# Kernel optimization log

Measured on AMD Instinct MI355X. Metric: run time of the kernel, lower is better.

## Reference

```python
import jax, jax.numpy as jnp
import numpy as np

HEAD_DIM = 64
N_HEADS = 64
N_KV = 8
Q_MULT = N_HEADS // N_KV  # 8
HIDDEN = 2880
SEQ = 1024
BATCH = 2
SLIDING_WINDOW = 128  # layer_idx=0 -> window active
ROPE_THETA = 150000.0
SCALING = 32.0
NTK_ALPHA = 1.0
NTK_BETA = 32.0
INIT_CTX = 4096
EPS = 1e-5


def _rope_caches(seq_len):
    # YaRN rotary caches (static numpy precompute, as in the source module)
    steps = np.arange(0, HEAD_DIM, 2, dtype=np.float32)
    freq = np.power(np.float32(ROPE_THETA), steps / np.float32(HEAD_DIM))
    concentration = np.float32(0.1) * np.log(np.float32(SCALING)) + 1.0
    d_half = np.float32(HEAD_DIM / 2.0)
    log_base = np.log(np.float32(ROPE_THETA))
    low = d_half * np.log(np.float32(INIT_CTX) / (np.float32(NTK_BETA) * np.float32(2.0 * np.pi))) / log_base
    high = d_half * np.log(np.float32(INIT_CTX) / (np.float32(NTK_ALPHA) * np.float32(2.0 * np.pi))) / log_base
    ramp = (np.arange(HEAD_DIM // 2, dtype=np.float32) - low) / (high - low)
    mask = 1.0 - np.clip(ramp, 0.0, 1.0)
    inv_freq = (1.0 / (np.float32(SCALING) * freq)) * (1.0 - mask) + (1.0 / freq) * mask
    pos = np.arange(seq_len, dtype=np.float32)
    freqs = np.einsum('i,j->ij', pos, inv_freq.astype(np.float32))
    cos = (np.cos(freqs) * concentration).astype(np.float32)
    sin = (np.sin(freqs) * concentration).astype(np.float32)
    return jnp.asarray(cos), jnp.asarray(sin)


def _apply_rotary(t, cos, sin):
    # t: (B, S, ..., head_dim); cos/sin: (S, head_dim//2). Rotate-half style.
    shape = (1, t.shape[1]) + (1,) * (t.ndim - 3) + (cos.shape[-1],)
    c = cos.reshape(shape)
    s = sin.reshape(shape)
    first, second = jnp.split(t, 2, axis=-1)
    return jnp.concatenate([first * c - second * s, second * c + first * s], axis=-1)


def setup_inputs() -> dict:
    key = jax.random.key(0)
    ks = jax.random.split(key, 6)
    qkv_dim = (N_HEADS + 2 * N_KV) * HEAD_DIM  # 5120
    return {
        'x': jax.random.normal(ks[0], (BATCH, SEQ, HIDDEN), dtype=jnp.float32),
        'norm_w': jnp.ones((HIDDEN,), dtype=jnp.float32),
        'qkv_w': jax.random.normal(ks[1], (qkv_dim, HIDDEN), dtype=jnp.float32) * 0.02,
        'qkv_b': jax.random.normal(ks[2], (qkv_dim,), dtype=jnp.float32) * 0.02,
        'out_w': jax.random.normal(ks[3], (HIDDEN, N_HEADS * HEAD_DIM), dtype=jnp.float32) * 0.02,
        'out_b': jax.random.normal(ks[4], (HIDDEN,), dtype=jnp.float32) * 0.02,
        'sinks': jax.random.normal(ks[5], (N_HEADS,), dtype=jnp.float32),
    }


def reference(x, norm_w, qkv_w, qkv_b, out_w, out_b, sinks):
    B, S, _ = x.shape
    # RMSNorm (fp32 accumulation)
    xf = x.astype(jnp.float32)
    rms = jnp.mean(xf * xf, axis=-1, keepdims=True)
    t = (xf * jax.lax.rsqrt(rms + EPS) * norm_w).astype(x.dtype)
    # QKV projection (fp32 accumulation)
    qkv = jnp.matmul(t.astype(jnp.float32), qkv_w.T) + qkv_b
    q_dim = N_HEADS * HEAD_DIM
    kv_dim = N_KV * HEAD_DIM
    q = qkv[..., :q_dim].reshape(B, S, N_KV, Q_MULT, HEAD_DIM)
    k = qkv[..., q_dim:q_dim + kv_dim].reshape(B, S, N_KV, HEAD_DIM)
    v = qkv[..., q_dim + kv_dim:].reshape(B, S, N_KV, HEAD_DIM)
    # YaRN rotary embedding
    cos, sin = _rope_caches(S)
    q = _apply_rotary(q, cos, sin)
    k = _apply_rotary(k, cos, sin)
    # causal + sliding-window mask
    neg_inf = jnp.float32(-jnp.inf)
    mask = jnp.triu(jnp.full((S, S), neg_inf, dtype=jnp.float32), k=1)
    mask = mask + jnp.tril(jnp.full((S, S), neg_inf, dtype=jnp.float32), k=-SLIDING_WINDOW)
    sm_scale = jnp.float32(1.0 / np.sqrt(HEAD_DIM))
    # GQA attention with sink logits
    logits = jnp.einsum('bqhmd,bkhd->bhmqk', q, k) * sm_scale + mask[None, None, None]
    sink = jnp.broadcast_to(sinks.reshape(1, N_KV, Q_MULT, 1, 1), (B, N_KV, Q_MULT, S, 1))
    logits = jnp.concatenate([logits, sink], axis=-1)
    w = jax.nn.softmax(logits, axis=-1)[..., :-1]  # drop sink column
    attn = jnp.einsum('bhmqk,bkhd->bqhmd', w, v).reshape(B, S, N_HEADS * HEAD_DIM)
    # output projection (fp32 accumulation) + residual
    out = jnp.matmul(attn, out_w.T) + out_b
    return x + out
```

## Files before the change

### kernel.cpp

```cpp
#include <hip/hip_runtime.h>

typedef unsigned short ushort_t;
typedef __attribute__((ext_vector_type(8))) short short8;
typedef __attribute__((ext_vector_type(8))) __bf16 bf16x8;
typedef __attribute__((ext_vector_type(4))) float float4v;
typedef __attribute__((ext_vector_type(4))) unsigned int uint4v;

__device__ __forceinline__ float bf2f(ushort_t u) {
    unsigned int v = ((unsigned int)u) << 16;
    return __builtin_bit_cast(float, v);
}
__device__ __forceinline__ ushort_t f2bf(float f) {
    unsigned int u = __builtin_bit_cast(unsigned int, f);
    unsigned int lsb = (u >> 16) & 1u;
    u += 0x7fffu + lsb;
    return (ushort_t)(u >> 16);
}
__device__ __forceinline__ uint4v pack8(const ushort_t* r) {
    uint4v u;
#pragma unroll
    for (int i = 0; i < 4; ++i)
        u[i] = (unsigned int)r[2 * i] | ((unsigned int)r[2 * i + 1] << 16);
    return u;
}
__device__ __forceinline__ void unpack8(uint4v u, float* f) {
#pragma unroll
    for (int i = 0; i < 4; ++i) {
        unsigned int x = u[i];
        f[2 * i] = __builtin_bit_cast(float, x << 16);
        f[2 * i + 1] = __builtin_bit_cast(float, x & 0xffff0000u);
    }
}
__device__ __forceinline__ uint4v ld8f32_bf(const float* p) {
    float4v a = *(const float4v*)p;
    float4v b = *(const float4v*)(p + 4);
    ushort_t r[8];
#pragma unroll
    for (int j = 0; j < 4; ++j) { r[j] = f2bf(a[j]); r[4 + j] = f2bf(b[j]); }
    return pack8(r);
}

#if __has_builtin(__builtin_amdgcn_global_load_lds)
#define HAVE_GLDS 1
__device__ __forceinline__ void glds16(const ushort_t* gp, ushort_t* lp) {
    __builtin_amdgcn_global_load_lds((const __attribute__((address_space(1))) void*)gp,
                                     (__attribute__((address_space(3))) void*)lp, 16, 0, 0);
}
#else
#define HAVE_GLDS 0
#endif

template <typename V>
__device__ __forceinline__ auto mfma_sel(V a, V b, float4v c, int)
    -> decltype(__builtin_amdgcn_mfma_f32_16x16x32_bf16(a, b, c, 0, 0, 0)) {
    return __builtin_amdgcn_mfma_f32_16x16x32_bf16(a, b, c, 0, 0, 0);
}
template <typename V>
__device__ __forceinline__ float4v mfma_sel(V a, V b, float4v c, long) {
    return __builtin_amdgcn_mfma_f32_16x16x32_bf16(__builtin_bit_cast(bf16x8, a),
                                                   __builtin_bit_cast(bf16x8, b), c, 0, 0, 0);
}
__device__ __forceinline__ float4v mfma_bf16(short8 a, short8 b, float4v c) {
    return mfma_sel(a, b, c, 0);
}

__device__ __forceinline__ float wave_sum(float v) {
#pragma unroll
    for (int o = 32; o; o >>= 1) v += __shfl_xor(v, o);
    return v;
}

#define HIDDEN 2880
#define NTOK 2048
#define QKV_DIM 5120
#define ATTN_DIM 4096
#define SM_SCALE 0.125f

#define ROPE_STEP 0.37244970540869975f
#define ROPE_CONC 1.3465735902799727f
#define ROPE_LOW 8.092890725542669f
#define ROPE_INVDEN 0.10745959154836568f

__device__ __forceinline__ float rope_invfreq(int j) {
    float invf = __expf(-(float)j * ROPE_STEP);
    float ramp = ((float)j - ROPE_LOW) * ROPE_INVDEN;
    float mask = 1.f - fminf(fmaxf(ramp, 0.f), 1.f);
    return invf * ((1.f - mask) * 0.03125f + mask);
}

__global__ __launch_bounds__(256) void prep_kernel(const float* __restrict__ x,
                                                   const float* __restrict__ wgt,
                                                   ushort_t* __restrict__ tout,
                                                   const float* __restrict__ a,
                                                   ushort_t* __restrict__ ao, int na8,
                                                   const float* __restrict__ b,
                                                   ushort_t* __restrict__ bo, int nb8) {
    const int tid = threadIdx.x;
    __shared__ float red[4];
    if (blockIdx.x < NTOK) {
        const int tok = blockIdx.x;
        const float* xr = x + (size_t)tok * HIDDEN;
        float v[16];
        float ss = 0.f;
#pragma unroll
        for (int i = 0; i < 2; ++i) {
            int c = tid + i * 256;
            if (c < 360) {
                float4v va = *(const float4v*)(xr + c * 8);
                float4v vb = *(const float4v*)(xr + c * 8 + 4);
#pragma unroll
                for (int j = 0; j < 4; ++j) { v[i * 8 + j] = va[j]; v[i * 8 + 4 + j] = vb[j]; }
#pragma unroll
                for (int j = 0; j < 8; ++j) ss += v[i * 8 + j] * v[i * 8 + j];
            }
        }
        ss = wave_sum(ss);
        if ((tid & 63) == 0) red[tid >> 6] = ss;
        __syncthreads();
        float scale = rsqrtf((red[0] + red[1] + red[2] + red[3]) * (1.f / 2880.f) + 1e-5f);
#pragma unroll
        for (int i = 0; i < 2; ++i) {
            int c = tid + i * 256;
            if (c < 360) {
                float4v wa = *(const float4v*)(wgt + c * 8);
                float4v wb = *(const float4v*)(wgt + c * 8 + 4);
                ushort_t r[8];
#pragma unroll
                for (int j = 0; j < 4; ++j) {
                    r[j] = f2bf(v[i * 8 + j] * scale * wa[j]);
                    r[4 + j] = f2bf(v[i * 8 + 4 + j] * scale * wb[j]);
                }
                *(uint4v*)(tout + (size_t)tok * HIDDEN + c * 8) = pack8(r);
            }
        }
    } else {
        int idx = (blockIdx.x - NTOK) * 256 + tid;
        if (idx < na8) {
            *(uint4v*)(ao + (size_t)idx * 8) = ld8f32_bf(a + (size_t)idx * 8);
        } else {
            int j = idx - na8;
            if (j < nb8) *(uint4v*)(bo + (size_t)j * 8) = ld8f32_bf(b + (size_t)j * 8);
        }
    }
}

__global__ __launch_bounds__(256) void rmsnorm_kernel(const float* __restrict__ x,
                                                      const float* __restrict__ wgt,
                                                      ushort_t* __restrict__ out) {
    const int tok = blockIdx.x, tid = threadIdx.x;
    const float* xr = x + (size_t)tok * HIDDEN;
    float v[16];
    float ss = 0.f;
#pragma unroll
    for (int i = 0; i < 2; ++i) {
        int c = tid + i * 256;
        if (c < 360) {
            float4v a = *(const float4v*)(xr + c * 8);
            float4v b = *(const float4v*)(xr + c * 8 + 4);
#pragma unroll
            for (int j = 0; j < 4; ++j) { v[i * 8 + j] = a[j]; v[i * 8 + 4 + j] = b[j]; }
#pragma unroll
            for (int j = 0; j < 8; ++j) ss += v[i * 8 + j] * v[i * 8 + j];
        }
    }
    ss = wave_sum(ss);
    __shared__ float red[4];
    if ((tid & 63) == 0) red[tid >> 6] = ss;
    __syncthreads();
    float scale = rsqrtf((red[0] + red[1] + red[2] + red[3]) * (1.f / 2880.f) + 1e-5f);
#pragma unroll
    for (int i = 0; i < 2; ++i) {
        int c = tid + i * 256;
        if (c < 360) {
            float4v wa = *(const float4v*)(wgt + c * 8);
            float4v wb = *(const float4v*)(wgt + c * 8 + 4);
            ushort_t r[8];
#pragma unroll
            for (int j = 0; j < 4; ++j) {
                r[j] = f2bf(v[i * 8 + j] * scale * wa[j]);
                r[4 + j] = f2bf(v[i * 8 + 4 + j] * scale * wb[j]);
            }
            *(uint4v*)(out + (size_t)tok * HIDDEN + c * 8) = pack8(r);
        }
    }
}

template <int BN, bool RESID, bool OUTF32, bool BF16B>
__global__ __launch_bounds__(256) void gemm_kernel(const ushort_t* __restrict__ A,
                                                   const void* __restrict__ B,
                                                   const float* __restrict__ bias,
                                                   const float* __restrict__ resid,
                                                   void* __restrict__ Cout, int M, int N, int K) {
    constexpr int BM = 128, BK = 64;
    constexpr bool GL = BF16B && (HAVE_GLDS != 0);
    constexpr int LDT = GL ? 64 : 72;
    constexpr int NBUF = GL ? 2 : 1;
    static_assert(BN == 160 || BN == 128 || BN == 96 || BN == 64, "");
    __shared__ __align__(16) ushort_t As[NBUF][BM * LDT];
    __shared__ __align__(16) ushort_t Bs[NBUF][BN * LDT];

    const int nbx = gridDim.x;
    int wg = blockIdx.y * nbx + blockIdx.x;
    {
        const int nwg = nbx * gridDim.y;
        const int cpx = nwg >> 3;
        wg = (wg & 7) * cpx + (wg >> 3);
    }
    const int m0 = (wg / nbx) * BM;
    const int n0 = (wg % nbx) * BN;
    const int tid = threadIdx.x;
    const int w = tid >> 6, lane = tid & 63;
    const int quad = lane >> 4, l16 = lane & 15;

    constexpr int WN = BN / 2;
    constexpr int NI = WN / 16;
    const int wm = (w >> 1) * 64;
    const int wn = (w & 1) * WN;

    float4v acc[4][NI];
#pragma unroll
    for (int i = 0; i < 4; ++i)
#pragma unroll
        for (int j = 0; j < NI; ++j) acc[i][j] = (float4v){0.f, 0.f, 0.f, 0.f};

    const int nk = K / BK;

#if HAVE_GLDS
    if constexpr (GL) {
        constexpr int NAI = BM / 32;
        constexpr int NBI = BN / 32;
        const ushort_t* Bp = (const ushort_t*)B;
        const ushort_t* agp[NAI];
        const ushort_t* bgp[NBI];
        ushort_t* alp[2][NAI];
        ushort_t* blp[2][NBI];
#pragma unroll
        for (int i = 0; i < NAI; ++i) {
            int sb = (w * NAI + i) * 64;
            int s = sb + lane, r = s >> 3, p = s & 7, c = p ^ (r & 7);
            agp[i] = A + (size_t)(m0 + r) * K + c * 8;
            alp[0][i] = &As[0][sb * 8];
            alp[1][i] = &As[1][sb * 8];
        }
#pragma unroll
        for (int i = 0; i < NBI; ++i) {
            int sb = (w * NBI + i) * 64;
            int s = sb + lane, r = s >> 3, p = s & 7, c = p ^ (r & 7);
            bgp[i] = Bp + (size_t)(n0 + r) * K + c * 8;
            blp[0][i] = &Bs[0][sb * 8];
            blp[1][i] = &Bs[1][sb * 8];
        }
#pragma unroll
        for (int i = 0; i < NAI; ++i) glds16(agp[i], alp[0][i]);
#pragma unroll
        for (int i = 0; i < NBI; ++i) glds16(bgp[i], blp[0][i]);
        __syncthreads();

        for (int kt = 0; kt < nk; ++kt) {
            const int cur = kt & 1;
            if (kt + 1 < nk) {
                const int k0 = (kt + 1) * BK;
#pragma unroll
                for (int i = 0; i < NAI; ++i) glds16(agp[i] + k0, alp[cur ^ 1][i]);
#pragma unroll
                for (int i = 0; i < NBI; ++i) glds16(bgp[i] + k0, blp[cur ^ 1][i]);
            }
            const ushort_t* Asb = As[cur];
            const ushort_t* Bsb = Bs[cur];
#pragma unroll
            for (int ks = 0; ks < 2; ++ks) {
                short8 af[4], bfr[NI];
#pragma unroll
                for (int mi = 0; mi < 4; ++mi) {
                    int row = wm + mi * 16 + l16;
                    af[mi] = *(const short8*)(Asb + row * LDT + ((ks * 4 + quad) ^ (row & 7)) * 8);
                }
#pragma unroll
                for (int ni = 0; ni < NI; ++ni) {
                    int row = wn + ni * 16 + l16;
                    bfr[ni] = *(const short8*)(Bsb + row * LDT + ((ks * 4 + quad) ^ (row & 7)) * 8);
                }
#pragma unroll
                for (int mi = 0; mi < 4; ++mi)
#pragma unroll
                    for (int ni = 0; ni < NI; ++ni)
                        acc[mi][ni] = mfma_bf16(af[mi], bfr[ni], acc[mi][ni]);
            }
            __syncthreads();
        }
    } else
#endif
    {
        constexpr int ACH = BM * BK / 8 / 256;
        constexpr int BCH = BN * BK / 8 / 256;
        uint4v areg[ACH], breg[BCH];
#pragma unroll
        for (int i = 0; i < ACH; ++i) {
            int c = tid + i * 256, r = c >> 3, col = c & 7;
            areg[i] = *(const uint4v*)(A + (size_t)(m0 + r) * K + col * 8);
        }
#pragma unroll
        for (int i = 0; i < BCH; ++i) {
            int c = tid + i * 256, r = c >> 3, col = c & 7;
            if constexpr (BF16B)
                breg[i] = *(const uint4v*)((const ushort_t*)B + (size_t)(n0 + r) * K + col * 8);
            else
                breg[i] = ld8f32_bf((const float*)B + (size_t)(n0 + r) * K + col * 8);
        }
        for (int kt = 0; kt < nk; ++kt) {
            __syncthreads();
#pragma unroll
            for (int i = 0; i < ACH; ++i) {
                int c = tid + i * 256, r = c >> 3, col = c & 7;
                *(uint4v*)(&As[0][r * LDT + col * 8]) = areg[i];
            }
#pragma unroll
            for (int i = 0; i < BCH; ++i) {
                int c = tid + i * 256, r = c >> 3, col = c & 7;
                *(uint4v*)(&Bs[0][r * LDT + col * 8]) = breg[i];
            }
            __syncthreads();
            if (kt + 1 < nk) {
                const int k0 = (kt + 1) * BK;
#pragma unroll
                for (int i = 0; i < ACH; ++i) {
                    int c = tid + i * 256, r = c >> 3, col = c & 7;
                    areg[i] = *(const uint4v*)(A + (size_t)(m0 + r) * K + k0 + col * 8);
                }
#pragma unroll
                for (int i = 0; i < BCH; ++i) {
                    int c = tid + i * 256, r = c >> 3, col = c & 7;
                    if constexpr (BF16B)
                        breg[i] = *(const uint4v*)((const ushort_t*)B + (size_t)(n0 + r) * K + k0 + col * 8);
                    else
                        breg[i] = ld8f32_bf((const float*)B + (size_t)(n0 + r) * K + k0 + col * 8);
                }
            }
#pragma unroll
            for (int ks = 0; ks < 2; ++ks) {
                short8 af[4], bfr[NI];
#pragma unroll
                for (int mi = 0; mi < 4; ++mi)
                    af[mi] = *(const short8*)(&As[0][(wm + mi * 16 + l16) * LDT + ks * 32 + quad * 8]);
#pragma unroll
                for (int ni = 0; ni < NI; ++ni)
                    bfr[ni] = *(const short8*)(&Bs[0][(wn + ni * 16 + l16) * LDT + ks * 32 + quad * 8]);
#pragma unroll
                for (int mi = 0; mi < 4; ++mi)
#pragma unroll
                    for (int ni = 0; ni < NI; ++ni)
                        acc[mi][ni] = mfma_bf16(af[mi], bfr[ni], acc[mi][ni]);
            }
        }
    }

#pragma unroll
    for (int ni = 0; ni < NI; ++ni) {
        int gc = n0 + wn + ni * 16 + l16;
        float bv = bias[gc];
#pragma unroll
        for (int mi = 0; mi < 4; ++mi) {
#pragma unroll
            for (int r = 0; r < 4; ++r) {
                int gr = m0 + wm + mi * 16 + quad * 4 + r;
                float vv = acc[mi][ni][r] + bv;
                if constexpr (RESID) vv += resid[(size_t)gr * N + gc];
                if constexpr (OUTF32) ((float*)Cout)[(size_t)gr * N + gc] = vv;
                else ((ushort_t*)Cout)[(size_t)gr * N + gc] = f2bf(vv);
            }
        }
    }
}

__global__ __launch_bounds__(256, 2) void attn_mfma_kernel(const ushort_t* __restrict__ qkv,
                                                           const float* __restrict__ sinks,
                                                           ushort_t* __restrict__ attnbuf) {
    constexpr int LDK = 72, LDV = 200, LDP = 200;
    __shared__ __align__(16) ushort_t Ks[192 * LDK];
    __shared__ __align__(16) ushort_t Vt[64 * LDV];
    __shared__ __align__(16) ushort_t Pb[4][16 * LDP];

    const int qc = blockIdx.x, kvh = blockIdx.y >> 1, half = blockIdx.y & 1, b = blockIdx.z;
    const int tid = threadIdx.x;
    const int w = tid >> 6, lane = tid & 63;
    const int quad = lane >> 4, l16 = lane & 15;
    const int w0 = qc * 64 - 127;

    {
        float invfK[8];
#pragma unroll
        for (int jj = 0; jj < 8; ++jj) invfK[jj] = rope_invfreq((tid & 3) * 8 + jj);
        for (int c = tid; c < 192 * 4; c += 256) {
            int row = c >> 2, col4 = c & 3;
            int pos = w0 + row;
            pos = pos < 0 ? 0 : (pos > 1023 ? 1023 : pos);
            size_t gk = ((size_t)(b * 1024 + pos)) * QKV_DIM + 4096 + kvh * 64 + col4 * 8;
            uint4v u1 = *(const uint4v*)(qkv + gk);
            uint4v u2 = *(const uint4v*)(qkv + gk + 32);
            float f1[8], f2[8];
            unpack8(u1, f1);
            unpack8(u2, f2);
            float s = (float)pos;
            ushort_t r1[8], r2[8];
#pragma unroll
            for (int jj = 0; jj < 8; ++jj) {
                float ang = s * invfK[jj];
                float cc = __cosf(ang) * ROPE_CONC;
                float sn = __sinf(ang) * ROPE_CONC;
                r1[jj] = f2bf(f1[jj] * cc - f2[jj] * sn);
                r2[jj] = f2bf(f2[jj] * cc + f1[jj] * sn);
            }
            *(uint4v*)(Ks + row * LDK + col4 * 8) = pack8(r1);
            *(uint4v*)(Ks + row * LDK + (col4 + 4) * 8) = pack8(r2);
        }
    }
    for (int c = tid; c < 192 * 8; c += 256) {
        int row = c >> 3, col8 = c & 7;
        int pos = w0 + row;
        pos = pos < 0 ? 0 : (pos > 1023 ? 1023 : pos);
        size_t gv = ((size_t)(b * 1024 + pos)) * QKV_DIM + 4608 + kvh * 64 + col8 * 8;
        uint4v vv = *(const uint4v*)(qkv + gv);
        ushort_t vs[8];
#pragma unroll
        for (int i = 0; i < 4; ++i) {
            vs[2 * i] = (ushort_t)(vv[i] & 0xffffu);
            vs[2 * i + 1] = (ushort_t)(vv[i] >> 16);
        }
#pragma unroll
        for (int j = 0; j < 8; ++j) Vt[(col8 * 8 + j) * LDV + row] = vs[j];
    }
    __syncthreads();

    ushort_t* Pw = Pb[w];
    const int h = kvh * 8 + half * 4 + w;
    const float sink_f = sinks[h];

    float invfQ[8];
#pragma unroll
    for (int jj = 0; jj < 8; ++jj) invfQ[jj] = rope_invfreq(quad * 8 + jj);

    for (int p = 0; p < 2; ++p) {
        short8 Vf[5][4];
#pragma unroll
        for (int j = 0; j < 5; ++j)
#pragma unroll
            for (int nv = 0; nv < 4; ++nv)
                Vf[j][nv] = *(const short8*)(Vt + (nv * 16 + l16) * LDV + (p + j) * 32 + quad * 8);

#pragma unroll
        for (int qq = 0; qq < 2; ++qq) {
            const int qtile = 2 * p + qq;
            const int tokb = b * 1024 + qc * 64 + qtile * 16;

            short8 qf[2];
            {
                const ushort_t* qp = qkv + ((size_t)(tokb + l16)) * QKV_DIM + h * 64 + quad * 8;
                uint4v u1 = *(const uint4v*)qp;
                uint4v u2 = *(const uint4v*)(qp + 32);
                float f1[8], f2[8];
                unpack8(u1, f1);
                unpack8(u2, f2);
                float s = (float)((tokb + l16) & 1023);
                ushort_t r1[8], r2[8];
#pragma unroll
                for (int jj = 0; jj < 8; ++jj) {
                    float ang = s * invfQ[jj];
                    float cc = __cosf(ang) * ROPE_CONC;
                    float sn = __sinf(ang) * ROPE_CONC;
                    r1[jj] = f2bf(f1[jj] * cc - f2[jj] * sn);
                    r2[jj] = f2bf(f2[jj] * cc + f1[jj] * sn);
                }
                qf[0] = __builtin_bit_cast(short8, pack8(r1));
                qf[1] = __builtin_bit_cast(short8, pack8(r2));
            }

            float4v acc[9];
#pragma unroll
            for (int j = 0; j < 9; ++j) acc[j] = (float4v){0.f, 0.f, 0.f, 0.f};
            __builtin_amdgcn_s_setprio(1);
#pragma unroll
            for (int j = 0; j < 9; ++j) {
                const int nt = qtile + j;
#pragma unroll
                for (int ks = 0; ks < 2; ++ks) {
                    short8 kf = *(const short8*)(Ks + (nt * 16 + l16) * LDK + ks * 32 + quad * 8);
                    acc[j] = mfma_bf16(qf[ks], kf, acc[j]);
                }
            }
            __builtin_amdgcn_s_setprio(0);

            const int ntz = qq ? (qtile - 1) : (qtile + 9);

            float linv[4];
#pragma unroll
            for (int r = 0; r < 4; ++r) {
                const int ql = qtile * 16 + quad * 4 + r;
                float e[9];
                float mx = -1e30f;
#pragma unroll
                for (int j = 0; j < 9; ++j) {
                    int row_k = (qtile + j) * 16 + l16;
                    bool valid = (row_k >= ql) && (row_k <= ql + 127) && (w0 + row_k >= 0);
                    float s = valid ? acc[j][r] * SM_SCALE : -1e30f;
                    e[j] = s;
                    mx = fmaxf(mx, s);
                }
#pragma unroll
                for (int o = 1; o < 16; o <<= 1) mx = fmaxf(mx, __shfl_xor(mx, o));
                float M = fmaxf(mx, sink_f);
                float ls = 0.f;
#pragma unroll
                for (int j = 0; j < 9; ++j) {
                    float ev = (e[j] > -1e29f) ? __expf(e[j] - M) : 0.f;
                    e[j] = ev;
                    ls += ev;
                }
#pragma unroll
                for (int o = 1; o < 16; o <<= 1) ls += __shfl_xor(ls, o);
                linv[r] = 1.f / (ls + __expf(sink_f - M));
#pragma unroll
                for (int j = 0; j < 9; ++j)
                    Pw[(quad * 4 + r) * LDP + (qtile + j) * 16 + l16] = f2bf(e[j]);
                Pw[(quad * 4 + r) * LDP + ntz * 16 + l16] = 0;
            }

            float4v accO[4];
#pragma unroll
            for (int nv = 0; nv < 4; ++nv) accO[nv] = (float4v){0.f, 0.f, 0.f, 0.f};
            __builtin_amdgcn_s_setprio(1);
#pragma unroll
            for (int j = 0; j < 5; ++j) {
                short8 pf = *(const short8*)(Pw + l16 * LDP + (p + j) * 32 + quad * 8);
#pragma unroll
                for (int nv = 0; nv < 4; ++nv) accO[nv] = mfma_bf16(pf, Vf[j][nv], accO[nv]);
            }
            __builtin_amdgcn_s_setprio(0);

#pragma unroll
            for (int r = 0; r < 4; ++r) {
                size_t ob = ((size_t)(tokb + quad * 4 + r)) * ATTN_DIM + h * 64 + l16;
#pragma unroll
                for (int nv = 0; nv < 4; ++nv)
                    attnbuf[ob + nv * 16] = f2bf(accO[nv][r] * linv[r]);
            }
        }
    }
}

extern "C" void kernel_launch(void* const* d_in, const int* in_sizes, int n_in,
                              void* d_out, int out_size, void* d_ws, size_t ws_size,
                              hipStream_t stream) {
    const float* x = (const float*)d_in[0];
    const float* norm_w = (const float*)d_in[1];
    const float* qkv_w = (const float*)d_in[2];
    const float* qkv_b = (const float*)d_in[3];
    const float* out_w = (const float*)d_in[4];
    const float* out_b = (const float*)d_in[5];
    const float* sinks = (const float*)d_in[6];
    float* outp = (float*)d_out;
    char* ws = (char*)d_ws;

    if (ws_size >= 86000000ull) {
        ushort_t* qkvbuf = (ushort_t*)ws;
        ushort_t* qkv_w_bf = (ushort_t*)(ws + 20971520);
        ushort_t* attnbuf = (ushort_t*)(ws + 20971520);
        ushort_t* out_w_bf = (ushort_t*)(ws + 50462720);
        ushort_t* Tbuf = (ushort_t*)d_out;

        prep_kernel<<<NTOK + 12960, 256, 0, stream>>>(x, norm_w, Tbuf, qkv_w, qkv_w_bf,
                                                      1843200, out_w, out_w_bf, 1474560);
        gemm_kernel<160, false, false, true><<<dim3(32, 16), 256, 0, stream>>>(
            Tbuf, qkv_w_bf, qkv_b, nullptr, qkvbuf, NTOK, QKV_DIM, HIDDEN);
        attn_mfma_kernel<<<dim3(16, 16, 2), 256, 0, stream>>>(qkvbuf, sinks, attnbuf);
        gemm_kernel<96, true, true, true><<<dim3(30, 16), 256, 0, stream>>>(
            attnbuf, out_w_bf, out_b, x, outp, NTOK, HIDDEN, ATTN_DIM);
    } else {
        ushort_t* qkvbuf = (ushort_t*)ws;
        ushort_t* attnbuf = (ushort_t*)(ws + 20971520);
        ushort_t* Tbuf = (ushort_t*)d_out;

        rmsnorm_kernel<<<NTOK, 256, 0, stream>>>(x, norm_w, Tbuf);
        gemm_kernel<128, false, false, false><<<dim3(40, 16), 256, 0, stream>>>(
            Tbuf, qkv_w, qkv_b, nullptr, qkvbuf, NTOK, QKV_DIM, HIDDEN);
        attn_mfma_kernel<<<dim3(16, 16, 2), 256, 0, stream>>>(qkvbuf, sinks, attnbuf);
        gemm_kernel<96, true, true, false><<<dim3(30, 16), 256, 0, stream>>>(
            attnbuf, out_w, out_b, x, outp, NTOK, HIDDEN, ATTN_DIM);
    }
}
```

Before: 308.7 us.

## Load B fragments directly into registers for output-projection GEMM

Adds a BREG variant of the GEMM in which each wave loads its B-operand MFMA fragments straight from global memory into registers, double-buffered across k-tiles. A still goes through LDS via async global-to-LDS copies. Only the output projection GEMM uses it. This removes B's LDS traffic and LDS footprint, at the cost of more register pressure and uncoalesced row-strided global loads of B that each wave issues on its own.

```diff
diff --git a/kernel.cpp b/kernel.cpp
--- a/kernel.cpp
+++ b/kernel.cpp
@@ -185,7 +185,7 @@
     }
 }
 
-template <int BN, bool RESID, bool OUTF32, bool BF16B>
+template <int BN, bool RESID, bool OUTF32, bool BF16B, bool BREG = false>
 __global__ __launch_bounds__(256) void gemm_kernel(const ushort_t* __restrict__ A,
                                                    const void* __restrict__ B,
                                                    const float* __restrict__ bias,
@@ -193,11 +193,13 @@
                                                    void* __restrict__ Cout, int M, int N, int K) {
     constexpr int BM = 128, BK = 64;
     constexpr bool GL = BF16B && (HAVE_GLDS != 0);
+    constexpr bool USE_BREG = BREG && GL;
     constexpr int LDT = GL ? 64 : 72;
     constexpr int NBUF = GL ? 2 : 1;
     static_assert(BN == 160 || BN == 128 || BN == 96 || BN == 64, "");
+    constexpr int BS_ELEMS = USE_BREG ? 8 : BN * LDT;
     __shared__ __align__(16) ushort_t As[NBUF][BM * LDT];
-    __shared__ __align__(16) ushort_t Bs[NBUF][BN * LDT];
+    __shared__ __align__(16) ushort_t Bs[NBUF][BS_ELEMS];
 
     const int nbx = gridDim.x;
     int wg = blockIdx.y * nbx + blockIdx.x;
@@ -226,7 +228,77 @@
     const int nk = K / BK;
 
 #if HAVE_GLDS
-    if constexpr (GL) {
+    if constexpr (USE_BREG) {
+        constexpr int NAI = BM / 32;
+        const ushort_t* Bp = (const ushort_t*)B;
+        const ushort_t* agp[NAI];
+        ushort_t* alp[2][NAI];
+#pragma unroll
+        for (int i = 0; i < NAI; ++i) {
+            int sb = (w * NAI + i) * 64;
+            int s = sb + lane, r = s >> 3, p = s & 7, c = p ^ (r & 7);
+            agp[i] = A + (size_t)(m0 + r) * K + c * 8;
+            alp[0][i] = &As[0][sb * 8];
+            alp[1][i] = &As[1][sb * 8];
+        }
+        const ushort_t* brow[NI];
+#pragma unroll
+        for (int ni = 0; ni < NI; ++ni)
+            brow[ni] = Bp + (size_t)(n0 + wn + ni * 16 + l16) * K + quad * 8;
+
+        uint4v bregA[2][NI], bregB[2][NI];
+
+#define LOAD_B(dst, ktv)                                                       \
+    {                                                                          \
+        const int kb = (ktv) * BK;                                             \
+        _Pragma("unroll") for (int ks = 0; ks < 2; ++ks)                       \
+            _Pragma("unroll") for (int ni = 0; ni < NI; ++ni)                  \
+                dst[ks][ni] = *(const uint4v*)(brow[ni] + kb + ks * 32);       \
+    }
+#define COMPUTE_TILE(bufi, bsrc)                                               \
+    {                                                                          \
+        const ushort_t* Asb = As[bufi];                                        \
+        _Pragma("unroll") for (int ks = 0; ks < 2; ++ks) {                     \
+            short8 af[4], bfr[NI];                                             \
+            _Pragma("unroll") for (int mi = 0; mi < 4; ++mi) {                 \
+                int row = wm + mi * 16 + l16;                                  \
+                af[mi] = *(const short8*)(Asb + row * LDT +                    \
+                                          (((ks * 4 + quad) ^ (row & 7)) * 8));\
+            }                                                                  \
+            _Pragma("unroll") for (int ni = 0; ni < NI; ++ni)                  \
+                bfr[ni] = __builtin_bit_cast(short8, bsrc[ks][ni]);            \
+            _Pragma("unroll") for (int mi = 0; mi < 4; ++mi)                   \
+                _Pragma("unroll") for (int ni = 0; ni < NI; ++ni)              \
+                    acc[mi][ni] = mfma_bf16(af[mi], bfr[ni], acc[mi][ni]);     \
+        }                                                                      \
+    }
+
+#pragma unroll
+        for (int i = 0; i < NAI; ++i) glds16(agp[i], alp[0][i]);
+        LOAD_B(bregA, 0);
+        __syncthreads();
+
+        for (int kt = 0; kt < nk; kt += 2) {
+            if (kt + 1 < nk) {
+                LOAD_B(bregB, kt + 1);
+                const int k0 = (kt + 1) * BK;
+#pragma unroll
+                for (int i = 0; i < NAI; ++i) glds16(agp[i] + k0, alp[1][i]);
+            }
+            COMPUTE_TILE(0, bregA);
+            __syncthreads();
+            if (kt + 2 < nk) {
+                LOAD_B(bregA, kt + 2);
+                const int k0 = (kt + 2) * BK;
+#pragma unroll
+                for (int i = 0; i < NAI; ++i) glds16(agp[i] + k0, alp[0][i]);
+            }
+            COMPUTE_TILE(1, bregB);
+            __syncthreads();
+        }
+#undef LOAD_B
+#undef COMPUTE_TILE
+    } else if constexpr (GL) {
         constexpr int NAI = BM / 32;
         constexpr int NBI = BN / 32;
         const ushort_t* Bp = (const ushort_t*)B;
@@ -317,7 +389,7 @@
 #pragma unroll
             for (int i = 0; i < BCH; ++i) {
                 int c = tid + i * 256, r = c >> 3, col = c & 7;
-                *(uint4v*)(&Bs[0][r * LDT + col * 8]) = breg[i];
+                *(uint4v*)(&Bs[0][(size_t)r * LDT + col * 8]) = breg[i];
             }
             __syncthreads();
             if (kt + 1 < nk) {
@@ -344,7 +416,7 @@
                     af[mi] = *(const short8*)(&As[0][(wm + mi * 16 + l16) * LDT + ks * 32 + quad * 8]);
 #pragma unroll
                 for (int ni = 0; ni < NI; ++ni)
-                    bfr[ni] = *(const short8*)(&Bs[0][(wn + ni * 16 + l16) * LDT + ks * 32 + quad * 8]);
+                    bfr[ni] = *(const short8*)(&Bs[0][(size_t)(wn + ni * 16 + l16) * LDT + ks * 32 + quad * 8]);
 #pragma unroll
                 for (int mi = 0; mi < 4; ++mi)
 #pragma unroll
@@ -572,7 +644,7 @@
         gemm_kernel<160, false, false, true><<<dim3(32, 16), 256, 0, stream>>>(
             Tbuf, qkv_w_bf, qkv_b, nullptr, qkvbuf, NTOK, QKV_DIM, HIDDEN);
         attn_mfma_kernel<<<dim3(16, 16, 2), 256, 0, stream>>>(qkvbuf, sinks, attnbuf);
-        gemm_kernel<96, true, true, true><<<dim3(30, 16), 256, 0, stream>>>(
+        gemm_kernel<96, true, true, true, true><<<dim3(30, 16), 256, 0, stream>>>(
             attnbuf, out_w_bf, out_b, x, outp, NTOK, HIDDEN, ATTN_DIM);
     } else {
         ushort_t* qkvbuf = (ushort_t*)ws;
```

New measurement: 363.3 us. 17.7% more time.

## Move out_w bf16 conversion into extra blocks of the attention kernel

Applied to the files above, without the earlier changes.

The fp32-to-bf16 conversion of the output projection weight moves out of the prep kernel into additional blocks appended to the attention grid. The attention launch has few blocks, so the conversion work can fill otherwise idle compute units while attention runs. This shortens the prep kernel's critical path. The cost is extra memory traffic competing with attention, plus a more complex kernel with an early-exit branch.

```diff
diff --git a/kernel.cpp b/kernel.cpp
--- a/kernel.cpp
+++ b/kernel.cpp
@@ -92,9 +92,7 @@
                                                    const float* __restrict__ wgt,
                                                    ushort_t* __restrict__ tout,
                                                    const float* __restrict__ a,
-                                                   ushort_t* __restrict__ ao, int na8,
-                                                   const float* __restrict__ b,
-                                                   ushort_t* __restrict__ bo, int nb8) {
+                                                   ushort_t* __restrict__ ao, int na8) {
     const int tid = threadIdx.x;
     __shared__ float red[4];
     if (blockIdx.x < NTOK) {
@@ -135,12 +133,7 @@
         }
     } else {
         int idx = (blockIdx.x - NTOK) * 256 + tid;
-        if (idx < na8) {
-            *(uint4v*)(ao + (size_t)idx * 8) = ld8f32_bf(a + (size_t)idx * 8);
-        } else {
-            int j = idx - na8;
-            if (j < nb8) *(uint4v*)(bo + (size_t)j * 8) = ld8f32_bf(b + (size_t)j * 8);
-        }
+        if (idx < na8) *(uint4v*)(ao + (size_t)idx * 8) = ld8f32_bf(a + (size_t)idx * 8);
     }
 }
 
@@ -317,7 +310,7 @@
 #pragma unroll
             for (int i = 0; i < BCH; ++i) {
                 int c = tid + i * 256, r = c >> 3, col = c & 7;
-                *(uint4v*)(&Bs[0][r * LDT + col * 8]) = breg[i];
+                *(uint4v*)(&Bs[0][(size_t)r * LDT + col * 8]) = breg[i];
             }
             __syncthreads();
             if (kt + 1 < nk) {
@@ -344,7 +337,7 @@
                     af[mi] = *(const short8*)(&As[0][(wm + mi * 16 + l16) * LDT + ks * 32 + quad * 8]);
 #pragma unroll
                 for (int ni = 0; ni < NI; ++ni)
-                    bfr[ni] = *(const short8*)(&Bs[0][(wn + ni * 16 + l16) * LDT + ks * 32 + quad * 8]);
+                    bfr[ni] = *(const short8*)(&Bs[0][(size_t)(wn + ni * 16 + l16) * LDT + ks * 32 + quad * 8]);
 #pragma unroll
                 for (int mi = 0; mi < 4; ++mi)
 #pragma unroll
@@ -372,13 +365,27 @@
     }
 }
 
+#define CONVX 45
 __global__ __launch_bounds__(256, 2) void attn_mfma_kernel(const ushort_t* __restrict__ qkv,
                                                            const float* __restrict__ sinks,
-                                                           ushort_t* __restrict__ attnbuf) {
+                                                           ushort_t* __restrict__ attnbuf,
+                                                           const float* __restrict__ ow,
+                                                           ushort_t* __restrict__ ow_bf) {
     constexpr int LDK = 72, LDV = 200, LDP = 200;
     __shared__ __align__(16) ushort_t Ks[192 * LDK];
     __shared__ __align__(16) ushort_t Vt[64 * LDV];
     __shared__ __align__(16) ushort_t Pb[4][16 * LDP];
+
+    if (blockIdx.x >= 16) {
+        const int conv_id = (blockIdx.x - 16) + CONVX * (blockIdx.y * 2 + blockIdx.z);
+        const int base = conv_id * 256 + threadIdx.x;
+#pragma unroll
+        for (int k = 0; k < 4; ++k) {
+            int idx = base + k * (CONVX * 32 * 256);
+            *(uint4v*)(ow_bf + (size_t)idx * 8) = ld8f32_bf(ow + (size_t)idx * 8);
+        }
+        return;
+    }
 
     const int qc = blockIdx.x, kvh = blockIdx.y >> 1, half = blockIdx.y & 1, b = blockIdx.z;
     const int tid = threadIdx.x;
@@ -567,11 +574,12 @@
         ushort_t* out_w_bf = (ushort_t*)(ws + 50462720);
         ushort_t* Tbuf = (ushort_t*)d_out;
 
-        prep_kernel<<<NTOK + 12960, 256, 0, stream>>>(x, norm_w, Tbuf, qkv_w, qkv_w_bf,
-                                                      1843200, out_w, out_w_bf, 1474560);
+        prep_kernel<<<NTOK + 7200, 256, 0, stream>>>(x, norm_w, Tbuf, qkv_w, qkv_w_bf,
+                                                     1843200);
         gemm_kernel<160, false, false, true><<<dim3(32, 16), 256, 0, stream>>>(
             Tbuf, qkv_w_bf, qkv_b, nullptr, qkvbuf, NTOK, QKV_DIM, HIDDEN);
-        attn_mfma_kernel<<<dim3(16, 16, 2), 256, 0, stream>>>(qkvbuf, sinks, attnbuf);
+        attn_mfma_kernel<<<dim3(16 + CONVX, 16, 2), 256, 0, stream>>>(
+            qkvbuf, sinks, attnbuf, out_w, out_w_bf);
         gemm_kernel<96, true, true, true><<<dim3(30, 16), 256, 0, stream>>>(
             attnbuf, out_w_bf, out_b, x, outp, NTOK, HIDDEN, ATTN_DIM);
     } else {
@@ -582,7 +590,8 @@
         rmsnorm_kernel<<<NTOK, 256, 0, stream>>>(x, norm_w, Tbuf);
         gemm_kernel<128, false, false, false><<<dim3(40, 16), 256, 0, stream>>>(
             Tbuf, qkv_w, qkv_b, nullptr, qkvbuf, NTOK, QKV_DIM, HIDDEN);
-        attn_mfma_kernel<<<dim3(16, 16, 2), 256, 0, stream>>>(qkvbuf, sinks, attnbuf);
+        attn_mfma_kernel<<<dim3(16, 16, 2), 256, 0, stream>>>(
+            qkvbuf, sinks, attnbuf, nullptr, nullptr);
         gemm_kernel<96, true, true, false><<<dim3(30, 16), 256, 0, stream>>>(
             attnbuf, out_w, out_b, x, outp, NTOK, HIDDEN, ATTN_DIM);
     }
```

After: 314.1 us. Within noise of the previous version (+1.8%).
